# Performance work log

Measured on AMD Instinct MI355X. Metric: run time of the kernel, lower is better.

The kernel has to match this reference:

```python
import jax, jax.numpy as jnp
import numpy as np

B, S, H, I, L, NH = 1, 256, 384, 1536, 2, 8

def _gelu(x):
    return jax.nn.gelu(x, approximate=False)  # torch nn.GELU default = exact erf

def _ln(x, g, b, eps=1e-5):
    m = x.mean(-1, keepdims=True)
    v = jnp.var(x, axis=-1, keepdims=True)
    return (x - m) / jnp.sqrt(v + eps) * g + b

def _mha(x, Wqkv, bqkv, Wo, bo):
    b_, s_, h_ = x.shape
    d = h_ // NH
    qkv = x @ Wqkv.T + bqkv  # [B,S,3H]
    q, k, v = jnp.split(qkv, 3, axis=-1)
    sp = lambda t: t.reshape(b_, s_, NH, d).transpose(0, 2, 1, 3)  # [B,NH,S,d]
    q, k, v = sp(q), sp(k), sp(v)
    att = jax.nn.softmax(jnp.einsum('bhqd,bhkd->bhqk', q * (1.0 / np.sqrt(d)), k), axis=-1)
    o = jnp.einsum('bhqk,bhkd->bhqd', att, v).transpose(0, 2, 1, 3).reshape(b_, s_, h_)
    return o @ Wo.T + bo

def _forward(hidden_states, Wqkv, bqkv, Wo, bo, W1, b1, W2, b2, g1, be1, g2, be2,
             Wbil, bbil, Wc1, bc1, Wc2, bc2, Wih, bih, Whh, bhh, Wp1, bp1, Wp2, bp2,
             Wout, bout, reasoning_steps):
    x = hidden_states
    rstate = jnp.zeros((x.shape[0], x.shape[-1]), x.dtype)
    cprobs, conts = [], []
    for _ in range(reasoning_steps):
        # symbolic reasoning layers (eval mode: dropout off)
        for l in range(L):
            x = _ln(x + _mha(x, Wqkv[l], bqkv[l], Wo[l], bo[l]), g1[l], be1[l])
            ff = _gelu(x @ W1[l].T + b1[l]) @ W2[l].T + b2[l]
            x = _ln(x + ff, g2[l], be2[l])
        # contradiction detector: bilinear over all token pairs
        tmp = jnp.einsum('bix,oxy->bioy', x, Wbil)            # [B,S,H,H]
        inter = jnp.einsum('bioy,bjy->bijo', tmp, x) + bbil   # [B,S,S,H]
        h1 = _gelu(inter @ Wc1.T + bc1)                       # [B,S,S,H]
        logits = jnp.einsum('bijh,h->bij', h1, Wc2[0]) + bc2[0]
        cprobs.append(jax.nn.sigmoid(logits))
        # recursive reasoning controller (GRUCell on mean-pooled states)
        pooled = x.mean(axis=1)
        gi = pooled @ Wih.T + bih
        gh = rstate @ Whh.T + bhh
        ir, iz, inn = jnp.split(gi, 3, axis=-1)
        hr, hz, hn = jnp.split(gh, 3, axis=-1)
        r = jax.nn.sigmoid(ir + hr)
        z = jax.nn.sigmoid(iz + hz)
        n = jnp.tanh(inn + r * hn)
        rstate = (1.0 - z) * n + z * rstate
        conts.append(jax.nn.sigmoid(_gelu(rstate @ Wp1.T + bp1) @ Wp2[0] + bp2[0]))
    final = x @ Wout.T + bout
    return final, jnp.stack(cprobs), jnp.stack(conts)

def setup_inputs():
    key = jax.random.key(0)
    ks = iter(jax.random.split(key, 40))
    rn = lambda shape, s=0.02: jax.random.normal(next(ks), shape, jnp.float32) * s
    return {
        'hidden_states': jax.random.normal(next(ks), (B, S, H), jnp.float32),
        'Wqkv': rn((L, 3 * H, H)), 'bqkv': jnp.zeros((L, 3 * H)),
        'Wo': rn((L, H, H)), 'bo': jnp.zeros((L, H)),
        'W1': rn((L, I, H)), 'b1': jnp.zeros((L, I)),
        'W2': rn((L, H, I)), 'b2': jnp.zeros((L, H)),
        'g1': jnp.ones((L, H)), 'be1': jnp.zeros((L, H)),
        'g2': jnp.ones((L, H)), 'be2': jnp.zeros((L, H)),
        'Wbil': rn((H, H, H)), 'bbil': jnp.zeros((H,)),
        'Wc1': rn((H, H)), 'bc1': jnp.zeros((H,)),
        'Wc2': rn((1, H)), 'bc2': jnp.zeros((1,)),
        'Wih': rn((3 * H, H)), 'bih': jnp.zeros((3 * H,)),
        'Whh': rn((3 * H, H)), 'bhh': jnp.zeros((3 * H,)),
        'Wp1': rn((H, H)), 'bp1': jnp.zeros((H,)),
        'Wp2': rn((1, H)), 'bp2': jnp.zeros((1,)),
        'Wout': rn((H, H)), 'bout': jnp.zeros((H,)),
        'reasoning_steps': 2,
    }

def reference(hidden_states, Wqkv, bqkv, Wo, bo, W1, b1, W2, b2, g1, be1, g2, be2,
              Wbil, bbil, Wc1, bc1, Wc2, bc2, Wih, bih, Whh, bhh, Wp1, bp1, Wp2, bp2,
              Wout, bout, reasoning_steps):
    return _forward(hidden_states, Wqkv, bqkv, Wo, bo, W1, b1, W2, b2, g1, be1, g2, be2,
                    Wbil, bbil, Wc1, bc1, Wc2, bc2, Wih, bih, Whh, bhh, Wp1, bp1, Wp2, bp2,
                    Wout, bout, reasoning_steps)
```

## Files before the change

kernel.cpp:

```cpp
#include <hip/hip_runtime.h>

typedef __attribute__((ext_vector_type(4))) float f32x4;
typedef __attribute__((ext_vector_type(8))) short s16x8;

#define DEVI __device__ __forceinline__

DEVI float b2f(short s) {
  union { float f; unsigned u; } v; v.u = ((unsigned)(unsigned short)s) << 16; return v.f;
}
DEVI short f2b(float f) {
  union { float f; unsigned u; } v; v.f = f;
  unsigned u = v.u;
  u += 0x7FFFu + ((u >> 16) & 1u);
  return (short)(u >> 16);
}
DEVI float gelu_f(float x) {
  float z2 = 1.5957691216f * x * (1.0f + 0.044715f * x * x);
  float e = __expf(z2);
  float th = 1.0f - 2.0f / (e + 1.0f);
  return 0.5f * x * (1.0f + th);
}
DEVI float sigm_f(float x) { return 1.0f / (1.0f + expf(-x)); }

DEVI void gld16(const short* g, const short* l) {
  __builtin_amdgcn_global_load_lds((const __attribute__((address_space(1))) void*)g,
                                   (__attribute__((address_space(3))) void*)l, 16, 0, 0);
}

template<bool BIAS, bool OUT_BF16>
__global__ __launch_bounds__(512)
void gemm256_k(const short* __restrict__ A, const short* __restrict__ B,
               const float* __restrict__ bias, void* __restrict__ Cv,
               int N, int K,
               long long sA, long long sB, long long sC)
{
  __shared__ short As[2][256 * 32];
  __shared__ short Bs[2][128 * 32];
  const int bz = blockIdx.z;
  const int n0 = blockIdx.x * 128;
  const int t = threadIdx.x, lane = t & 63, wave = t >> 6;
  const int wm = wave >> 1, wn = wave & 1;
  const short* Ab = A + bz * sA;
  const short* Bb = B + bz * sB;
  const int lr = lane >> 2;
  const int lc = (lane & 3) * 8;
  const int fr = lane & 15, fs = lane >> 4;

  f32x4 acc[4][4];
#pragma unroll
  for (int i = 0; i < 4; ++i)
#pragma unroll
    for (int j = 0; j < 4; ++j) acc[i][j] = f32x4{0.f, 0.f, 0.f, 0.f};

  auto stage = [&](int b, int k0) {
#pragma unroll
    for (int q = 0; q < 2; ++q)
      gld16(Ab + (long long)(q * 128 + wave * 16 + lr) * K + k0 + lc,
            &As[b][(q * 128 + wave * 16) * 32]);
    gld16(Bb + (long long)(n0 + wave * 16 + lr) * K + k0 + lc,
          &Bs[b][wave * 16 * 32]);
  };

  const int NT = K >> 5;
  stage(0, 0);
  __syncthreads();
  for (int tt = 0; tt < NT; ++tt) {
    const int cur = tt & 1;
    if (tt + 1 < NT) stage(cur ^ 1, (tt + 1) << 5);
    s16x8 af[4], bfv[4];
#pragma unroll
    for (int i = 0; i < 4; ++i) af[i]  = *(const s16x8*)&As[cur][(wm * 64 + i * 16 + fr) * 32 + fs * 8];
#pragma unroll
    for (int j = 0; j < 4; ++j) bfv[j] = *(const s16x8*)&Bs[cur][(wn * 64 + j * 16 + fr) * 32 + fs * 8];
#pragma unroll
    for (int i = 0; i < 4; ++i)
#pragma unroll
      for (int j = 0; j < 4; ++j)
        acc[i][j] = __builtin_amdgcn_mfma_f32_16x16x32_bf16(af[i], bfv[j], acc[i][j], 0, 0, 0);
    if (tt + 1 < NT) __syncthreads();
  }

#pragma unroll
  for (int i = 0; i < 4; ++i) {
    int rowb = wm * 64 + i * 16 + fs * 4;
#pragma unroll
    for (int j = 0; j < 4; ++j) {
      int col = n0 + wn * 64 + j * 16 + fr;
      float bb = BIAS ? bias[col] : 0.0f;
#pragma unroll
      for (int u = 0; u < 4; ++u) {
        float v = acc[i][j][u] + bb;
        long long off = bz * sC + (long long)(rowb + u) * N + col;
        if constexpr (OUT_BF16) ((short*)Cv)[off] = f2b(v);
        else                    ((float*)Cv)[off] = v;
      }
    }
  }
}

__global__ __launch_bounds__(512)
void h1log256_k(const short* __restrict__ inter, const short* __restrict__ Wc1b,
                const float* __restrict__ bc1, const float* __restrict__ Wc2,
                const float* __restrict__ bc2, float* __restrict__ outp)
{
  __shared__ short As[2][256 * 32];
  __shared__ short Bs[2][128 * 32];
  __shared__ float part[256][2];
  const int ib = blockIdx.x;
  const int t = threadIdx.x, lane = t & 63, wave = t >> 6;
  const int wm = wave >> 1, wn = wave & 1;
  const short* Ab = inter + (long long)ib * 98304;
  const int lr = lane >> 2;
  const int lc = (lane & 3) * 8;
  const int fr = lane & 15, fs = lane >> 4;

  float lp[16];
#pragma unroll
  for (int e = 0; e < 16; ++e) lp[e] = 0.f;

  for (int n0 = 0; n0 < 384; n0 += 128) {
    f32x4 acc[4][4];
#pragma unroll
    for (int i = 0; i < 4; ++i)
#pragma unroll
      for (int j = 0; j < 4; ++j) acc[i][j] = f32x4{0.f, 0.f, 0.f, 0.f};

    auto stage = [&](int b, int k0) {
#pragma unroll
      for (int q = 0; q < 2; ++q)
        gld16(Ab + (long long)(q * 128 + wave * 16 + lr) * 384 + k0 + lc,
              &As[b][(q * 128 + wave * 16) * 32]);
      gld16(Wc1b + (long long)(n0 + wave * 16 + lr) * 384 + k0 + lc,
            &Bs[b][wave * 16 * 32]);
    };

    stage(0, 0);
    __syncthreads();
    for (int tt = 0; tt < 12; ++tt) {
      const int cur = tt & 1;
      if (tt + 1 < 12) stage(cur ^ 1, (tt + 1) << 5);
      s16x8 af[4], bfv[4];
#pragma unroll
      for (int i = 0; i < 4; ++i) af[i]  = *(const s16x8*)&As[cur][(wm * 64 + i * 16 + fr) * 32 + fs * 8];
#pragma unroll
      for (int j = 0; j < 4; ++j) bfv[j] = *(const s16x8*)&Bs[cur][(wn * 64 + j * 16 + fr) * 32 + fs * 8];
#pragma unroll
      for (int i = 0; i < 4; ++i)
#pragma unroll
        for (int j = 0; j < 4; ++j)
          acc[i][j] = __builtin_amdgcn_mfma_f32_16x16x32_bf16(af[i], bfv[j], acc[i][j], 0, 0, 0);
      if (tt + 1 < 12) __syncthreads();
    }
#pragma unroll
    for (int i = 0; i < 4; ++i)
#pragma unroll
      for (int j = 0; j < 4; ++j) {
        int col = n0 + wn * 64 + j * 16 + fr;
        float w2 = Wc2[col], b1v = bc1[col];
#pragma unroll
        for (int u = 0; u < 4; ++u)
          lp[i * 4 + u] += gelu_f(acc[i][j][u] + b1v) * w2;
      }
    __syncthreads();
  }
#pragma unroll
  for (int m = 1; m < 16; m <<= 1)
#pragma unroll
    for (int e = 0; e < 16; ++e) lp[e] += __shfl_xor(lp[e], m);
  if (fr == 0) {
#pragma unroll
    for (int e = 0; e < 16; ++e)
      part[wm * 64 + (e >> 2) * 16 + fs * 4 + (e & 3)][wn] = lp[e];
  }
  __syncthreads();
  if (t < 256) outp[ib * 256 + t] = sigm_f(part[t][0] + part[t][1] + bc2[0]);
}

template<bool BIAS, bool GELU_ACT, bool OUT_BF16>
__global__ __launch_bounds__(256)
void gemm64_k(const short* __restrict__ A, const short* __restrict__ B,
              const float* __restrict__ bias, void* __restrict__ Cv,
              int M, int N, int K)
{
  __shared__ short As[2][64 * 32];
  __shared__ short Bs[2][64 * 32];
  const int n0 = blockIdx.x * 64;
  const int m0 = blockIdx.y * 64;
  const int t = threadIdx.x, lane = t & 63, wave = t >> 6;
  const int wm = wave >> 1, wn = wave & 1;
  const int srow = lane >> 2;
  const int scol = (lane & 3) * 8;
  const int fr = lane & 15, fs = lane >> 4;

  f32x4 acc[2][2];
#pragma unroll
  for (int i = 0; i < 2; ++i)
#pragma unroll
    for (int j = 0; j < 2; ++j) acc[i][j] = f32x4{0.f, 0.f, 0.f, 0.f};

  auto stage = [&](int b, int k0) {
    gld16(A + (long long)(m0 + wave * 16 + srow) * K + k0 + scol, &As[b][wave * 512]);
    gld16(B + (long long)(n0 + wave * 16 + srow) * K + k0 + scol, &Bs[b][wave * 512]);
  };

  const int NT = K >> 5;
  stage(0, 0);
  __syncthreads();
  for (int tt = 0; tt < NT; ++tt) {
    const int cur = tt & 1;
    if (tt + 1 < NT) stage(cur ^ 1, (tt + 1) << 5);
    s16x8 af[2], bfv[2];
#pragma unroll
    for (int i = 0; i < 2; ++i) af[i]  = *(const s16x8*)&As[cur][(wm * 32 + i * 16 + fr) * 32 + fs * 8];
#pragma unroll
    for (int j = 0; j < 2; ++j) bfv[j] = *(const s16x8*)&Bs[cur][(wn * 32 + j * 16 + fr) * 32 + fs * 8];
#pragma unroll
    for (int i = 0; i < 2; ++i)
#pragma unroll
      for (int j = 0; j < 2; ++j)
        acc[i][j] = __builtin_amdgcn_mfma_f32_16x16x32_bf16(af[i], bfv[j], acc[i][j], 0, 0, 0);
    if (tt + 1 < NT) __syncthreads();
  }

#pragma unroll
  for (int i = 0; i < 2; ++i) {
    int rowb = m0 + wm * 32 + i * 16 + fs * 4;
#pragma unroll
    for (int j = 0; j < 2; ++j) {
      int col = n0 + wn * 32 + j * 16 + fr;
      float bb = BIAS ? bias[col] : 0.0f;
#pragma unroll
      for (int u = 0; u < 4; ++u) {
        float v = acc[i][j][u] + bb;
        if constexpr (GELU_ACT) v = gelu_f(v);
        long long off = (long long)(rowb + u) * N + col;
        if constexpr (OUT_BF16) ((short*)Cv)[off] = f2b(v);
        else                    ((float*)Cv)[off] = v;
      }
    }
  }
}

__global__ __launch_bounds__(256)
void transpose_k(const float* __restrict__ W, short* __restrict__ WT)
{
  __shared__ short L[64 * 68];
  const int o  = blockIdx.z;
  const int x0 = blockIdx.x * 64, y0 = blockIdx.y * 64;
  const float* Wo = W  + (long long)o * 147456;
  short*      WTo = WT + (long long)o * 147456;
  const int t  = threadIdx.x;
  const int rr = t >> 4;
  const int cc = (t & 15) * 4;
#pragma unroll
  for (int q = 0; q < 4; ++q) {
    int xl = rr + 16 * q;
    float4 v = *(const float4*)(Wo + (x0 + xl) * 384 + y0 + cc);
    short4 p; p.x = f2b(v.x); p.y = f2b(v.y); p.z = f2b(v.z); p.w = f2b(v.w);
    *(short4*)&L[xl * 68 + cc] = p;
  }
  __syncthreads();
#pragma unroll
  for (int q = 0; q < 4; ++q) {
    int yl = rr + 16 * q;
    short4 p;
    p.x = L[(cc + 0) * 68 + yl];
    p.y = L[(cc + 1) * 68 + yl];
    p.z = L[(cc + 2) * 68 + yl];
    p.w = L[(cc + 3) * 68 + yl];
    *(short4*)(WTo + (y0 + yl) * 384 + x0 + cc) = p;
  }
}

__global__ __launch_bounds__(256)
void convall_k(const float* __restrict__ Wc1, const float* __restrict__ Wqkv,
               const float* __restrict__ Wo, const float* __restrict__ W1,
               const float* __restrict__ W2, const float* __restrict__ Wout,
               short* __restrict__ Dc1, short* __restrict__ Dqkv,
               short* __restrict__ Do, short* __restrict__ D1,
               short* __restrict__ D2, short* __restrict__ Dout)
{
  long long i4 = ((long long)blockIdx.x * 256 + threadIdx.x) * 4;
  const float* s; short* d; long long off;
  if      (i4 <  147456) { s = Wc1;  d = Dc1;  off = 0; }
  else if (i4 < 1032192) { s = Wqkv; d = Dqkv; off = 147456; }
  else if (i4 < 1327104) { s = Wo;   d = Do;   off = 1032192; }
  else if (i4 < 2506752) { s = W1;   d = D1;   off = 1327104; }
  else if (i4 < 3686400) { s = W2;   d = D2;   off = 2506752; }
  else if (i4 < 3833856) { s = Wout; d = Dout; off = 3686400; }
  else return;
  long long l = i4 - off;
  float4 v = *(const float4*)(s + l);
  short4 p; p.x = f2b(v.x); p.y = f2b(v.y); p.z = f2b(v.z); p.w = f2b(v.w);
  *(short4*)(d + l) = p;
}

__global__ __launch_bounds__(256)
void attn_k(const float* __restrict__ qkv, short* __restrict__ outb)
{
  __shared__ short Ks[256 * 48];
  __shared__ short Vs[256 * 48];
  __shared__ float Ps[32][258];
  const int h  = blockIdx.y;
  const int q0 = blockIdx.x * 32;
  const int t = threadIdx.x, lane = t & 63, wave = t >> 6;
  for (int idx = t; idx < 3072; idx += 256) {
    int j = idx / 12, d4 = (idx - (idx / 12) * 12) * 4;
    const float* base = qkv + j * 1152 + h * 48 + d4;
    float4 kv = *(const float4*)(base + 384);
    float4 vv = *(const float4*)(base + 768);
    short4 pk; pk.x = f2b(kv.x); pk.y = f2b(kv.y); pk.z = f2b(kv.z); pk.w = f2b(kv.w);
    short4 pv; pv.x = f2b(vv.x); pv.y = f2b(vv.y); pv.z = f2b(vv.z); pv.w = f2b(vv.w);
    *(short4*)&Ks[j * 48 + d4] = pk;
    *(short4*)&Vs[j * 48 + d4] = pv;
  }
  __syncthreads();
  const int part = lane & 7;
  const int rl   = wave * 8 + (lane >> 3);
  const int row  = q0 + rl;
  float q[48];
#pragma unroll
  for (int d = 0; d < 48; ++d) q[d] = qkv[row * 1152 + h * 48 + d] * 0.14433756729740644f;
  float mx = -1e30f;
  for (int jj = 0; jj < 32; ++jj) {
    int j = jj * 8 + part;
    float a = 0.f;
#pragma unroll
    for (int dd = 0; dd < 12; ++dd) {
      short4 kk = *(const short4*)&Ks[j * 48 + dd * 4];
      a += q[dd*4+0]*b2f(kk.x) + q[dd*4+1]*b2f(kk.y) + q[dd*4+2]*b2f(kk.z) + q[dd*4+3]*b2f(kk.w);
    }
    Ps[rl][j] = a;
    mx = fmaxf(mx, a);
  }
  mx = fmaxf(mx, __shfl_xor(mx, 1));
  mx = fmaxf(mx, __shfl_xor(mx, 2));
  mx = fmaxf(mx, __shfl_xor(mx, 4));
  float sum = 0.f;
  for (int jj = 0; jj < 32; ++jj) {
    int j = jj * 8 + part;
    float e = expf(Ps[rl][j] - mx);
    Ps[rl][j] = e;
    sum += e;
  }
  sum += __shfl_xor(sum, 1); sum += __shfl_xor(sum, 2); sum += __shfl_xor(sum, 4);
  const float inv = 1.f / sum;
  __syncthreads();
  float o[6] = {0.f, 0.f, 0.f, 0.f, 0.f, 0.f};
  const int vb = part * 6;
  for (int j = 0; j < 256; ++j) {
    float p = Ps[rl][j];
    int base = j * 48 + vb;
#pragma unroll
    for (int dd = 0; dd < 3; ++dd) {
      short2 vv = *(const short2*)&Vs[base + dd * 2];
      o[dd*2]   += p * b2f(vv.x);
      o[dd*2+1] += p * b2f(vv.y);
    }
  }
#pragma unroll
  for (int d = 0; d < 6; ++d) outb[row * 384 + h * 48 + vb + d] = f2b(o[d] * inv);
}

__global__ __launch_bounds__(128)
void ln_k(const float* __restrict__ x, const short* __restrict__ d,
          const float* __restrict__ g, const float* __restrict__ b,
          float* __restrict__ xo, short* __restrict__ xob)
{
  const int row = blockIdx.x, t = threadIdx.x;
  float v[3]; float s = 0.f, ss = 0.f;
#pragma unroll
  for (int i = 0; i < 3; ++i) {
    int c = t + 128 * i;
    float u = x[row * 384 + c] + b2f(d[row * 384 + c]);
    v[i] = u; s += u; ss += u * u;
  }
#pragma unroll
  for (int m = 1; m < 64; m <<= 1) { s += __shfl_xor(s, m); ss += __shfl_xor(ss, m); }
  __shared__ float sh[4];
  if ((t & 63) == 0) { sh[(t >> 6) * 2] = s; sh[(t >> 6) * 2 + 1] = ss; }
  __syncthreads();
  s = sh[0] + sh[2]; ss = sh[1] + sh[3];
  float mean = s * (1.f / 384.f);
  float var  = ss * (1.f / 384.f) - mean * mean;
  float rstd = rsqrtf(var + 1e-5f);
#pragma unroll
  for (int i = 0; i < 3; ++i) {
    int c = t + 128 * i;
    float y = (v[i] - mean) * rstd * g[c] + b[c];
    xo[row * 384 + c]  = y;
    xob[row * 384 + c] = f2b(y);
  }
}

__global__ void init_k(const float* __restrict__ hs, float* __restrict__ x,
                       short* __restrict__ xb, float* __restrict__ rstate)
{
  int i = blockIdx.x * 256 + threadIdx.x;
  if (i < 98304) { float v = hs[i]; x[i] = v; xb[i] = f2b(v); }
  if (i < 384) rstate[i] = 0.f;
}

__global__ __launch_bounds__(384)
void pool1_k(const float* __restrict__ x, float* __restrict__ partial)
{
  const int t = threadIdx.x, p = blockIdx.x;
  float s = 0.f;
  const float* xr = x + p * 32 * 384;
#pragma unroll 4
  for (int i = 0; i < 32; ++i) s += xr[i * 384 + t];
  partial[p * 384 + t] = s;
}

__global__ __launch_bounds__(256)
void gih_k(const float* __restrict__ Wih, const float* __restrict__ bih,
           const float* __restrict__ Whh, const float* __restrict__ bhh,
           const float* __restrict__ partial, const float* __restrict__ rstate,
           float* __restrict__ gi, float* __restrict__ gh)
{
  const int t = threadIdx.x, lane = t & 63, wave = t >> 6;
  const int r = blockIdx.x * 4 + wave;
  float a = 0.f, b = 0.f;
#pragma unroll
  for (int e = 0; e < 6; ++e) {
    int c = lane + 64 * e;
    float pc = 0.f;
#pragma unroll
    for (int p = 0; p < 8; ++p) pc += partial[p * 384 + c];
    pc *= (1.f / 256.f);
    a += Wih[r * 384 + c] * pc;
    b += Whh[r * 384 + c] * rstate[c];
  }
#pragma unroll
  for (int m = 1; m < 64; m <<= 1) { a += __shfl_xor(a, m); b += __shfl_xor(b, m); }
  if (lane == 0) { gi[r] = a + bih[r]; gh[r] = b + bhh[r]; }
}

__global__ __launch_bounds__(384)
void gru2_k(const float* __restrict__ gi, const float* __restrict__ gh,
            float* __restrict__ rstate, float* __restrict__ hnew)
{
  const int t = threadIdx.x;
  float r = sigm_f(gi[t] + gh[t]);
  float z = sigm_f(gi[384 + t] + gh[384 + t]);
  float n = tanhf(gi[768 + t] + r * gh[768 + t]);
  float h = (1.f - z) * n + z * rstate[t];
  rstate[t] = h;
  hnew[t] = h;
}

__global__ __launch_bounds__(256)
void p1_k(const float* __restrict__ Wp1, const float* __restrict__ bp1,
          const float* __restrict__ hnew, float* __restrict__ p1)
{
  const int t = threadIdx.x, lane = t & 63, wave = t >> 6;
  const int r = blockIdx.x * 4 + wave;
  float a = 0.f;
#pragma unroll
  for (int e = 0; e < 6; ++e) { int c = lane + 64 * e; a += Wp1[r * 384 + c] * hnew[c]; }
#pragma unroll
  for (int m = 1; m < 64; m <<= 1) a += __shfl_xor(a, m);
  if (lane == 0) p1[r] = gelu_f(a + bp1[r]);
}

__global__ __launch_bounds__(64)
void cont_k(const float* __restrict__ p1, const float* __restrict__ Wp2,
            const float* __restrict__ bp2, float* __restrict__ out_cont)
{
  const int lane = threadIdx.x;
  float a = 0.f;
#pragma unroll
  for (int e = 0; e < 6; ++e) { int c = lane + 64 * e; a += p1[c] * Wp2[c]; }
#pragma unroll
  for (int m = 1; m < 64; m <<= 1) a += __shfl_xor(a, m);
  if (lane == 0) out_cont[0] = sigm_f(a + bp2[0]);
}

extern "C" void kernel_launch(void* const* d_in, const int* in_sizes, int n_in,
                              void* d_out, int out_size, void* d_ws, size_t ws_size,
                              hipStream_t stream)
{
  const float* hs   = (const float*)d_in[0];
  const float* Wqkv = (const float*)d_in[1];
  const float* bqkv = (const float*)d_in[2];
  const float* Wo   = (const float*)d_in[3];
  const float* bo   = (const float*)d_in[4];
  const float* W1   = (const float*)d_in[5];
  const float* b1   = (const float*)d_in[6];
  const float* W2   = (const float*)d_in[7];
  const float* b2   = (const float*)d_in[8];
  const float* g1   = (const float*)d_in[9];
  const float* be1  = (const float*)d_in[10];
  const float* g2   = (const float*)d_in[11];
  const float* be2  = (const float*)d_in[12];
  const float* Wbil = (const float*)d_in[13];
  const float* bbil = (const float*)d_in[14];
  const float* Wc1  = (const float*)d_in[15];
  const float* bc1  = (const float*)d_in[16];
  const float* Wc2  = (const float*)d_in[17];
  const float* bc2  = (const float*)d_in[18];
  const float* Wih  = (const float*)d_in[19];
  const float* bih  = (const float*)d_in[20];
  const float* Whh  = (const float*)d_in[21];
  const float* bhh  = (const float*)d_in[22];
  const float* Wp1  = (const float*)d_in[23];
  const float* bp1  = (const float*)d_in[24];
  const float* Wp2  = (const float*)d_in[25];
  const float* bp2  = (const float*)d_in[26];
  const float* Wout = (const float*)d_in[27];
  const float* bout = (const float*)d_in[28];
  float* out = (float*)d_out;

  char* ws = (char*)d_ws;
  size_t off = 0;
  auto alloc = [&](size_t bytes) -> char* {
    char* p = ws + off; off += (bytes + 255) & ~(size_t)255; return p;
  };
  short* wbilT   = (short*)alloc(56623104ULL * 2);
  short* tmp     = (short*)alloc(256ULL * 147456 * 2);
  short* inter   = (short*)alloc(256ULL * 98304 * 2);
  float* x       = (float*)alloc(98304 * 4);
  short* xb      = (short*)alloc(98304 * 2);
  float* qkv     = (float*)alloc(294912 * 4);
  short* attnb   = (short*)alloc(98304 * 2);
  short* deltab  = (short*)alloc(98304 * 2);
  short* ff1b    = (short*)alloc(393216 * 2);
  float* rstate  = (float*)alloc(384 * 4);
  float* partial = (float*)alloc(8 * 384 * 4);
  float* gi      = (float*)alloc(1152 * 4);
  float* gh      = (float*)alloc(1152 * 4);
  float* hnew    = (float*)alloc(384 * 4);
  float* p1buf   = (float*)alloc(384 * 4);
  short* wc1b    = (short*)alloc(147456 * 2);
  short* wqkvb   = (short*)alloc(884736ULL * 2);
  short* wob     = (short*)alloc(294912ULL * 2);
  short* w1b     = (short*)alloc(1179648ULL * 2);
  short* w2b     = (short*)alloc(1179648ULL * 2);
  short* woutb   = (short*)alloc(147456 * 2);
  (void)ws_size; (void)in_sizes; (void)n_in; (void)out_size;

  dim3 B256(256);
  dim3 B512(512);

  init_k<<<dim3(384), B256, 0, stream>>>(hs, x, xb, rstate);
  transpose_k<<<dim3(6, 6, 384), B256, 0, stream>>>(Wbil, wbilT);
  convall_k<<<dim3(3744), B256, 0, stream>>>(Wc1, Wqkv, Wo, W1, W2, Wout,
                                             wc1b, wqkvb, wob, w1b, w2b, woutb);

  for (int s = 0; s < 2; ++s) {
    for (int l = 0; l < 2; ++l) {
      gemm64_k<true, false, false><<<dim3(18, 4), B256, 0, stream>>>(
          xb, wqkvb + l * 442368, bqkv + l * 1152, qkv, 256, 1152, 384);
      attn_k<<<dim3(8, 8), B256, 0, stream>>>(qkv, attnb);
      gemm64_k<true, false, true><<<dim3(6, 4), B256, 0, stream>>>(
          attnb, wob + l * 147456, bo + l * 384, deltab, 256, 384, 384);
      ln_k<<<dim3(256), dim3(128), 0, stream>>>(x, deltab, g1 + l * 384, be1 + l * 384, x, xb);
      gemm64_k<true, true, true><<<dim3(24, 4), B256, 0, stream>>>(
          xb, w1b + l * 589824, b1 + l * 1536, ff1b, 256, 1536, 384);
      gemm64_k<true, false, true><<<dim3(6, 4), B256, 0, stream>>>(
          ff1b, w2b + l * 589824, b2 + l * 384, deltab, 256, 384, 1536);
      ln_k<<<dim3(256), dim3(128), 0, stream>>>(x, deltab, g2 + l * 384, be2 + l * 384, x, xb);
    }
    gemm256_k<false, true><<<dim3(1152, 1, 1), B512, 0, stream>>>(
        xb, wbilT, (const float*)nullptr, tmp, 147456, 384, 0, 0, 0);
    gemm256_k<true, true><<<dim3(3, 1, 256), B512, 0, stream>>>(
        xb, tmp, bbil, inter, 384, 384, 0, 147456LL, 98304LL);
    h1log256_k<<<dim3(256), B512, 0, stream>>>(inter, wc1b, bc1, Wc2, bc2,
                                               out + 98304 + s * 65536);
    pool1_k<<<dim3(8), dim3(384), 0, stream>>>(x, partial);
    gih_k<<<dim3(288), B256, 0, stream>>>(Wih, bih, Whh, bhh, partial, rstate, gi, gh);
    gru2_k<<<dim3(1), dim3(384), 0, stream>>>(gi, gh, rstate, hnew);
    p1_k<<<dim3(96), B256, 0, stream>>>(Wp1, bp1, hnew, p1buf);
    cont_k<<<dim3(1), dim3(64), 0, stream>>>(p1buf, Wp2, bp2, out + 98304 + 131072 + s);
  }
  gemm64_k<true, false, false><<<dim3(6, 4), B256, 0, stream>>>(
      xb, woutb, bout, out, 256, 384, 384);
}
```

Baseline: 642.8 us.

## Double gemm64 K-tile to 64 with XOR-swizzled LDS layout

The generic 64x64 GEMM kernel now stages 64-wide K tiles instead of 32, halving the number of loop iterations and barriers per output tile. The LDS layout uses an XOR swizzle of the 16-byte column chunk by row to avoid bank conflicts on the fragment reads. This doubles shared memory per block, which may reduce occupancy, and requires K to be a multiple of 64.

Result: faster. 619.3 us (-3.6%).

```diff
diff --git a/kernel.cpp b/kernel.cpp
--- a/kernel.cpp
+++ b/kernel.cpp
@@ -182,14 +182,14 @@
               const float* __restrict__ bias, void* __restrict__ Cv,
               int M, int N, int K)
 {
-  __shared__ short As[2][64 * 32];
-  __shared__ short Bs[2][64 * 32];
+  __shared__ short As[2][64 * 64];
+  __shared__ short Bs[2][64 * 64];
   const int n0 = blockIdx.x * 64;
   const int m0 = blockIdx.y * 64;
   const int t = threadIdx.x, lane = t & 63, wave = t >> 6;
   const int wm = wave >> 1, wn = wave & 1;
-  const int srow = lane >> 2;
-  const int scol = (lane & 3) * 8;
+  const int srow = lane >> 3;
+  const int scol = ((lane & 7) ^ srow) * 8;
   const int fr = lane & 15, fs = lane >> 4;
 
   f32x4 acc[2][2];
@@ -199,26 +199,42 @@
     for (int j = 0; j < 2; ++j) acc[i][j] = f32x4{0.f, 0.f, 0.f, 0.f};
 
   auto stage = [&](int b, int k0) {
-    gld16(A + (long long)(m0 + wave * 16 + srow) * K + k0 + scol, &As[b][wave * 512]);
-    gld16(B + (long long)(n0 + wave * 16 + srow) * K + k0 + scol, &Bs[b][wave * 512]);
+#pragma unroll
+    for (int q = 0; q < 2; ++q) {
+      int c = wave * 2 + q;
+      gld16(A + (long long)(m0 + c * 8 + srow) * K + k0 + scol, &As[b][c * 512]);
+      gld16(B + (long long)(n0 + c * 8 + srow) * K + k0 + scol, &Bs[b][c * 512]);
+    }
   };
 
-  const int NT = K >> 5;
+  const int NT = K >> 6;
   stage(0, 0);
   __syncthreads();
   for (int tt = 0; tt < NT; ++tt) {
     const int cur = tt & 1;
-    if (tt + 1 < NT) stage(cur ^ 1, (tt + 1) << 5);
-    s16x8 af[2], bfv[2];
-#pragma unroll
-    for (int i = 0; i < 2; ++i) af[i]  = *(const s16x8*)&As[cur][(wm * 32 + i * 16 + fr) * 32 + fs * 8];
-#pragma unroll
-    for (int j = 0; j < 2; ++j) bfv[j] = *(const s16x8*)&Bs[cur][(wn * 32 + j * 16 + fr) * 32 + fs * 8];
-#pragma unroll
-    for (int i = 0; i < 2; ++i)
-#pragma unroll
-      for (int j = 0; j < 2; ++j)
-        acc[i][j] = __builtin_amdgcn_mfma_f32_16x16x32_bf16(af[i], bfv[j], acc[i][j], 0, 0, 0);
+    if (tt + 1 < NT) stage(cur ^ 1, (tt + 1) << 6);
+    s16x8 af[2][2], bfv[2][2];
+#pragma unroll
+    for (int i = 0; i < 2; ++i) {
+      int row = wm * 32 + i * 16 + fr;
+#pragma unroll
+      for (int s = 0; s < 2; ++s)
+        af[i][s] = *(const s16x8*)&As[cur][row * 64 + (((s * 4 + fs) ^ (fr & 7)) * 8)];
+    }
+#pragma unroll
+    for (int j = 0; j < 2; ++j) {
+      int row = wn * 32 + j * 16 + fr;
+#pragma unroll
+      for (int s = 0; s < 2; ++s)
+        bfv[j][s] = *(const s16x8*)&Bs[cur][row * 64 + (((s * 4 + fs) ^ (fr & 7)) * 8)];
+    }
+#pragma unroll
+    for (int s = 0; s < 2; ++s)
+#pragma unroll
+      for (int i = 0; i < 2; ++i)
+#pragma unroll
+        for (int j = 0; j < 2; ++j)
+          acc[i][j] = __builtin_amdgcn_mfma_f32_16x16x32_bf16(af[i][s], bfv[j][s], acc[i][j], 0, 0, 0);
     if (tt + 1 < NT) __syncthreads();
   }
 
```
